# Optimization experiments

Hardware: AMD Instinct MI355X
Metric: run time of the kernel (lower is better)

Reference implementation:

```python
import jax, jax.numpy as jnp
import numpy as np

B, T, C = 8, 2048, 1024
NEG_BIG = -1e30  # exp(NEG_BIG - row_max) underflows to exactly 0 in fp32


def setup_inputs() -> dict:
    key = jax.random.key(0)
    k1, k2 = jax.random.split(key)
    x = jax.random.normal(k1, (B, T, C), dtype=jnp.float32)
    # nn.Linear weight, shape [out, in]; forward computes x @ W^T
    W_H = jax.random.normal(k2, (C, C), dtype=jnp.float32) * (1.0 / np.sqrt(C))
    return {"x": x, "W_H": W_H}


def reference(x, W_H):
    Tdim = x.shape[1]
    xH = jnp.einsum('btc,dc->btd', x, W_H)          # H(x) = x @ W^T, [B,T,C]
    scores = jnp.einsum('btc,bsc->bts', x, xH)       # bilinear scores, [B,T,T]
    # tril_plus_one=True -> strictly-lower-triangular mask (diagonal=-1)
    mask = jnp.tril(jnp.ones((Tdim, Tdim), dtype=bool), k=-1)
    scores = jnp.where(mask, scores, NEG_BIG)
    wei = jax.nn.softmax(scores, axis=-1)            # fully-masked rows -> uniform, zeroed below
    all_masked = ~mask.any(axis=-1)                  # [T], True for row 0
    wei = jnp.where(all_masked[None, :, None], 0.0, wei)
    out = jnp.einsum('bts,bsc->btc', wei, xH)
    return -out
```

## Files before the change

### kernel.cpp

```cpp
#include <hip/hip_runtime.h>
#include <stdint.h>

#define Bn 8
#define Tn 2048
#define Cn 1024
#define Mn (Bn * Tn)
#define NTRI 136

typedef __attribute__((ext_vector_type(4))) float f32x4;
typedef _Float16 f16;
typedef __attribute__((ext_vector_type(8))) _Float16 f16x8;
typedef uint16_t u16;
typedef uint32_t u32;

static __device__ __forceinline__ u16 f2h(float f) {
  union { f16 h; u16 u; } c; c.h = (f16)f; return c.u;
}
static __device__ __forceinline__ f32x4 mfmaH(f16x8 a, f16x8 b, f32x4 c) {
  return __builtin_amdgcn_mfma_f32_16x16x32_f16(a, b, c, 0, 0, 0);
}
static __device__ __forceinline__ void gld16(const void* g, void* l) {
  __builtin_amdgcn_global_load_lds(
      (const __attribute__((address_space(1))) u32*)g,
      (__attribute__((address_space(3))) u32*)l, 16, 0, 0);
}

__global__ __launch_bounds__(256) void ksplitW(const float* __restrict__ s,
                                               u16* __restrict__ hi) {
  size_t i = ((size_t)blockIdx.x * 256 + threadIdx.x) * 8;
  float4 a = *(const float4*)(s + i), b = *(const float4*)(s + i + 4);
  float f[8] = {a.x, a.y, a.z, a.w, b.x, b.y, b.z, b.w};
  union { u16 u[8]; uint4 v; } H;
#pragma unroll
  for (int j = 0; j < 8; ++j) H.u[j] = f2h(f[j]);
  *(uint4*)(hi + i) = H.v;
}

__global__ __launch_bounds__(256) void ksplitX(const float* __restrict__ s,
                                               u16* __restrict__ hi,
                                               u16* __restrict__ lo) {
  size_t i = ((size_t)blockIdx.x * 256 + threadIdx.x) * 8;
  float4 a = *(const float4*)(s + i), b = *(const float4*)(s + i + 4);
  float f[8] = {a.x, a.y, a.z, a.w, b.x, b.y, b.z, b.w};
  union { u16 u[8]; uint4 v; } H, L;
#pragma unroll
  for (int j = 0; j < 8; ++j) {
    f16 h = (f16)f[j];
    union { f16 h; u16 u; } ch; ch.h = h;
    H.u[j] = ch.u;
    L.u[j] = f2h(f[j] - (float)h);
  }
  *(uint4*)(hi + i) = H.v;
  *(uint4*)(lo + i) = L.v;
}

__global__ __launch_bounds__(256) void k1_xh(const u16* __restrict__ x_h,
                                             const u16* __restrict__ W_h,
                                             u16* __restrict__ xh) {
  __shared__ __align__(16) u16 Ah[8192], Bh[8192];
  const int tid = threadIdx.x;
  const int m0 = blockIdx.x * 128, n0 = blockIdx.y * 128;
  const int wave = tid >> 6, lane = tid & 63;
  const int wrow = (wave >> 1) * 64, wcol = (wave & 1) * 64;
  const int quad = lane >> 4, l16 = lane & 15;

  f32x4 acc[4][4] = {};

  for (int k0 = 0; k0 < Cn; k0 += 64) {
#pragma unroll
    for (int i = 0; i < 4; ++i) {
      int chunk = i * 256 + tid;
      int kk = chunk >> 9, row = (chunk >> 2) & 127, c8 = (chunk & 3) * 8;
      gld16(x_h + (size_t)(m0 + row) * Cn + k0 + kk * 32 + c8, Ah + chunk * 8);
      gld16(W_h + (size_t)(n0 + row) * Cn + k0 + kk * 32 + c8, Bh + chunk * 8);
    }
    __syncthreads();
#pragma unroll
    for (int kk = 0; kk < 2; ++kk) {
      f16x8 a[4], b[4];
#pragma unroll
      for (int i = 0; i < 4; ++i) {
        a[i] = *(const f16x8*)(Ah + kk * 4096 + (wrow + i * 16 + l16) * 32 + quad * 8);
        b[i] = *(const f16x8*)(Bh + kk * 4096 + (wcol + i * 16 + l16) * 32 + quad * 8);
      }
#pragma unroll
      for (int mi = 0; mi < 4; ++mi)
#pragma unroll
        for (int ni = 0; ni < 4; ++ni)
          acc[mi][ni] = mfmaH(a[mi], b[ni], acc[mi][ni]);
    }
    __syncthreads();
  }
#pragma unroll
  for (int mi = 0; mi < 4; ++mi)
#pragma unroll
    for (int ni = 0; ni < 4; ++ni)
#pragma unroll
      for (int r = 0; r < 4; ++r) {
        int row = wrow + mi * 16 + quad * 4 + r;
        int col = wcol + ni * 16 + l16;
        xh[(size_t)(m0 + row) * Cn + n0 + col] = f2h(acc[mi][ni][r]);
      }
}

__global__ __launch_bounds__(256) void k2_scores(const u16* __restrict__ x_h,
                                                 const u16* __restrict__ x_l,
                                                 const u16* __restrict__ xh,
                                                 u16* __restrict__ P,
                                                 float* __restrict__ mt,
                                                 float* __restrict__ lt) {
  __shared__ __align__(16) union {
    struct { u16 Ah[4096], Al[4096], Bh[4096]; } s;
    struct { float Mrow[2][128]; float Lrow[2][128]; } e;
  } u;
  const int tid = threadIdx.x;
  const int bL = blockIdx.y;
  const int lin = blockIdx.x;
  int qt = 0;
  while ((qt + 1) * (qt + 2) / 2 <= lin) qt++;
  const int st = lin - qt * (qt + 1) / 2;
  const int t0 = qt * 128, s0 = st * 128;
  const int wave = tid >> 6, lane = tid & 63;
  const int wrow = (wave >> 1) * 64, wcol = (wave & 1) * 64;
  const int quad = lane >> 4, l16 = lane & 15;
  const int srow = tid >> 2, skc = (tid & 3) * 8;

  f32x4 acc[4][4] = {};
  const size_t aoff = ((size_t)bL * Tn + t0 + srow) * Cn + skc;
  const size_t boff = ((size_t)bL * Tn + s0 + srow) * Cn + skc;

  for (int k0 = 0; k0 < Cn; k0 += 32) {
#pragma unroll
    for (int i = 0; i < 2; ++i) {
      size_t ro = (size_t)i * 64 * Cn;
      int lo_ = i * 2048 + tid * 8;
      gld16(x_h + aoff + ro + k0, u.s.Ah + lo_);
      gld16(x_l + aoff + ro + k0, u.s.Al + lo_);
      gld16(xh + boff + ro + k0, u.s.Bh + lo_);
    }
    __syncthreads();
    f16x8 a_h[4], a_l[4], b_h[4];
#pragma unroll
    for (int i = 0; i < 4; ++i) {
      a_h[i] = *(const f16x8*)(u.s.Ah + (wrow + i * 16 + l16) * 32 + quad * 8);
      a_l[i] = *(const f16x8*)(u.s.Al + (wrow + i * 16 + l16) * 32 + quad * 8);
      b_h[i] = *(const f16x8*)(u.s.Bh + (wcol + i * 16 + l16) * 32 + quad * 8);
    }
#pragma unroll
    for (int mi = 0; mi < 4; ++mi)
#pragma unroll
      for (int ni = 0; ni < 4; ++ni) {
        acc[mi][ni] = mfmaH(a_h[mi], b_h[ni], acc[mi][ni]);
        acc[mi][ni] = mfmaH(a_l[mi], b_h[ni], acc[mi][ni]);
      }
    __syncthreads();
  }

  float rm[4][4];
#pragma unroll
  for (int mi = 0; mi < 4; ++mi)
#pragma unroll
    for (int r = 0; r < 4; ++r) {
      int row = wrow + mi * 16 + quad * 4 + r;
      float m = -1e30f;
#pragma unroll
      for (int ni = 0; ni < 4; ++ni) {
        int col = wcol + ni * 16 + l16;
        if (s0 + col >= t0 + row) acc[mi][ni][r] = -1e30f;
        m = fmaxf(m, acc[mi][ni][r]);
      }
      m = fmaxf(m, __shfl_xor(m, 1));
      m = fmaxf(m, __shfl_xor(m, 2));
      m = fmaxf(m, __shfl_xor(m, 4));
      m = fmaxf(m, __shfl_xor(m, 8));
      rm[mi][r] = m;
    }
  if (l16 == 0) {
#pragma unroll
    for (int mi = 0; mi < 4; ++mi)
#pragma unroll
      for (int r = 0; r < 4; ++r)
        u.e.Mrow[wave & 1][wrow + mi * 16 + quad * 4 + r] = rm[mi][r];
  }
  __syncthreads();
  float rs[4][4];
#pragma unroll
  for (int mi = 0; mi < 4; ++mi)
#pragma unroll
    for (int r = 0; r < 4; ++r) {
      int row = wrow + mi * 16 + quad * 4 + r;
      float m2 = fmaxf(u.e.Mrow[0][row], u.e.Mrow[1][row]);
      float s = 0.f;
#pragma unroll
      for (int ni = 0; ni < 4; ++ni) {
        int col = wcol + ni * 16 + l16;
        float p = (s0 + col < t0 + row) ? __expf(acc[mi][ni][r] - m2) : 0.0f;
        acc[mi][ni][r] = p;
        s += p;
      }
      s += __shfl_xor(s, 1);
      s += __shfl_xor(s, 2);
      s += __shfl_xor(s, 4);
      s += __shfl_xor(s, 8);
      rs[mi][r] = s;
      rm[mi][r] = m2;
    }
  if (l16 == 0) {
#pragma unroll
    for (int mi = 0; mi < 4; ++mi)
#pragma unroll
      for (int r = 0; r < 4; ++r)
        u.e.Lrow[wave & 1][wrow + mi * 16 + quad * 4 + r] = rs[mi][r];
  }
  __syncthreads();
  if ((wave & 1) == 0 && l16 == 0) {
#pragma unroll
    for (int mi = 0; mi < 4; ++mi)
#pragma unroll
      for (int r = 0; r < 4; ++r) {
        int row = wrow + mi * 16 + quad * 4 + r;
        size_t rI = (size_t)bL * Tn + t0 + row;
        mt[rI * 16 + st] = rm[mi][r];
        lt[rI * 16 + st] = u.e.Lrow[0][row] + u.e.Lrow[1][row];
      }
  }
  const size_t pbase = (size_t)(bL * NTRI + lin) * 16384;
#pragma unroll
  for (int mi = 0; mi < 4; ++mi)
#pragma unroll
    for (int ni = 0; ni < 4; ++ni)
#pragma unroll
      for (int r = 0; r < 4; ++r) {
        int row = wrow + mi * 16 + quad * 4 + r;
        int col = wcol + ni * 16 + l16;
        P[pbase + row * 128 + col] = f2h(acc[mi][ni][r]);
      }
}

__global__ __launch_bounds__(256) void k3_stats(const float* __restrict__ mt,
                                                const float* __restrict__ lt,
                                                float* __restrict__ Mr,
                                                float* __restrict__ Li) {
  int r = blockIdx.x * 256 + threadIdx.x;
  int t = r & (Tn - 1);
  int nt = (t == 0) ? 0 : (((t - 1) >> 7) + 1);
  float M = -1e30f;
  for (int i = 0; i < nt; ++i) M = fmaxf(M, mt[(size_t)r * 16 + i]);
  float L = 0.f;
  for (int i = 0; i < nt; ++i) L += lt[(size_t)r * 16 + i] * __expf(mt[(size_t)r * 16 + i] - M);
  Mr[r] = M;
  Li[r] = (L > 0.f) ? 1.f / L : 0.f;
}

__global__ __launch_bounds__(256) void ktr(const u16* __restrict__ src,
                                           u16* __restrict__ dst) {
  __shared__ __align__(16) u16 S[128 * 136];
  const int t0 = blockIdx.x * 128, c0 = blockIdx.y * 128, b = blockIdx.z;
  const int tid = threadIdx.x;
#pragma unroll
  for (int i = 0; i < 8; ++i) {
    int chunk = tid + i * 256;
    int row = chunk >> 4, c8 = (chunk & 15) * 8;
    uint4 v = *(const uint4*)(src + ((size_t)b * Tn + t0 + row) * Cn + c0 + c8);
    *(uint4*)(S + row * 136 + c8) = v;
  }
  __syncthreads();
#pragma unroll
  for (int i = 0; i < 8; ++i) {
    int chunk = tid + i * 256;
    int crow = chunk >> 4, t8 = (chunk & 15) * 8;
    union { u16 s[8]; uint4 v; } o;
#pragma unroll
    for (int j = 0; j < 8; ++j) o.s[j] = S[(t8 + j) * 136 + crow];
    *(uint4*)(dst + ((size_t)b * Cn + c0 + crow) * Tn + t0 + t8) = o.v;
  }
}

__global__ __launch_bounds__(256) void k4_out(const u16* __restrict__ P,
                                              const u16* __restrict__ xhT,
                                              const float* __restrict__ mt,
                                              const float* __restrict__ Mr,
                                              const float* __restrict__ Li,
                                              float* __restrict__ out) {
  __shared__ __align__(16) u16 Ap[8192], Bp[8192];
  const int tid = threadIdx.x;
  const int tt = 15 - blockIdx.x;
  const int cn = blockIdx.y, bL = blockIdx.z;
  const int t0 = tt * 128, c0 = cn * 128;
  const int wave = tid >> 6, lane = tid & 63;
  const int wrow = (wave >> 1) * 64, wcol = (wave & 1) * 64;
  const int quad = lane >> 4, l16 = lane & 15;

  f32x4 acc[4][4] = {};
  size_t rI[4]; float MrL[4], LiL[4];
#pragma unroll
  for (int mi = 0; mi < 4; ++mi) {
    rI[mi] = (size_t)bL * Tn + t0 + wrow + mi * 16 + l16;
    MrL[mi] = Mr[rI[mi]];
    LiL[mi] = Li[rI[mi]];
  }
  const size_t bbase = ((size_t)bL * Cn + c0) * Tn;

  for (int st = 0; st <= tt; ++st) {
    f16 ah[4];
#pragma unroll
    for (int mi = 0; mi < 4; ++mi)
      ah[mi] = (f16)(__expf(mt[rI[mi] * 16 + st] - MrL[mi]) * LiL[mi]);
    const size_t pbase = (size_t)(bL * NTRI + tt * (tt + 1) / 2 + st) * 16384;
#pragma unroll 1
    for (int kl = 0; kl < 128; kl += 64) {
#pragma unroll
      for (int i = 0; i < 4; ++i) {
        int chunk = i * 256 + tid;
        int kk = chunk >> 9, row = (chunk >> 2) & 127, c8 = (chunk & 3) * 8;
        gld16(P + pbase + (size_t)row * 128 + kl + kk * 32 + c8, Ap + chunk * 8);
        gld16(xhT + bbase + (size_t)row * Tn + st * 128 + kl + kk * 32 + c8, Bp + chunk * 8);
      }
      __syncthreads();
#pragma unroll
      for (int kk = 0; kk < 2; ++kk) {
        f16x8 a[4], b[4];
#pragma unroll
        for (int i = 0; i < 4; ++i) {
          a[i] = *(const f16x8*)(Ap + kk * 4096 + (wrow + i * 16 + l16) * 32 + quad * 8);
          f16x8 sv;
#pragma unroll
          for (int j = 0; j < 8; ++j) sv[j] = ah[i];
          a[i] = a[i] * sv;
          b[i] = *(const f16x8*)(Bp + kk * 4096 + (wcol + i * 16 + l16) * 32 + quad * 8);
        }
#pragma unroll
        for (int mi = 0; mi < 4; ++mi)
#pragma unroll
          for (int ni = 0; ni < 4; ++ni)
            acc[mi][ni] = mfmaH(a[mi], b[ni], acc[mi][ni]);
      }
      __syncthreads();
    }
  }
#pragma unroll
  for (int mi = 0; mi < 4; ++mi)
#pragma unroll
    for (int ni = 0; ni < 4; ++ni)
#pragma unroll
      for (int r = 0; r < 4; ++r) {
        int row = wrow + mi * 16 + quad * 4 + r;
        int col = wcol + ni * 16 + l16;
        out[((size_t)bL * Tn + t0 + row) * Cn + c0 + col] = -acc[mi][ni][r];
      }
}

extern "C" void kernel_launch(void* const* d_in, const int* in_sizes, int n_in,
                              void* d_out, int out_size, void* d_ws, size_t ws_size,
                              hipStream_t stream) {
  (void)in_sizes; (void)n_in; (void)out_size;
  const float* x = (const float*)d_in[0];
  const float* W = (const float*)d_in[1];
  float* out = (float*)d_out;

  const size_t FULL_NEED = 3ull * Mn * Cn * 2 + (size_t)Bn * NTRI * 16384 * 2 +
                           (size_t)Cn * Cn * 2 + 2ull * Mn * 16 * 4 + 2ull * Mn * 4;
  const int nch = (ws_size >= FULL_NEED) ? 1 : 2;
  const int nb = Bn / nch;
  const size_t rowsC = (size_t)nb * Tn;
  const size_t sA = rowsC * Cn * 2;

  char* p = (char*)d_ws;
  u16* x_h = (u16*)p; p += sA;
  u16* xLT = (u16*)p; p += sA;
  u16* xh  = (u16*)p; p += sA;
  u16* Pp  = (u16*)p; p += (size_t)nb * NTRI * 16384 * 2;
  u16* W_h = (u16*)p; p += (size_t)Cn * Cn * 2;
  float* mt = (float*)p; p += rowsC * 16 * 4;
  float* lt = (float*)p; p += rowsC * 16 * 4;
  float* Mr = (float*)p; p += rowsC * 4;
  float* Li = (float*)p; p += rowsC * 4;

  dim3 blk(256);
  ksplitW<<<dim3(Cn * Cn / 2048), blk, 0, stream>>>(W, W_h);
  for (int c = 0; c < nch; ++c) {
    const float* xc = x + (size_t)c * rowsC * Cn;
    float* oc = out + (size_t)c * rowsC * Cn;
    ksplitX<<<dim3((u32)(rowsC * Cn / 2048)), blk, 0, stream>>>(xc, x_h, xLT);
    k1_xh<<<dim3((u32)(rowsC / 128), Cn / 128), blk, 0, stream>>>(x_h, W_h, xh);
    k2_scores<<<dim3(NTRI, nb), blk, 0, stream>>>(x_h, xLT, xh, Pp, mt, lt);
    k3_stats<<<dim3((u32)(rowsC / 256)), blk, 0, stream>>>(mt, lt, Mr, Li);
    ktr<<<dim3(Tn / 128, Cn / 128, nb), blk, 0, stream>>>(xh, xLT);
    k4_out<<<dim3(16, Cn / 128, nb), blk, 0, stream>>>(Pp, xLT, mt, Mr, Li, oc);
  }
}
```

Baseline: 427.6 us.

## Widen score kernel tiles to 128x256 with 512 threads sharing A loads

The causal score kernel now computes 128x256 tiles per block using 8 waves, so each query-row A tile (hi and lo halves) is loaded once for two 128-wide key blocks. This cuts redundant global and LDS traffic for A and reduces block count from 136 to 72 per batch. The cost is some wasted MFMA work on the upper 128-column half of diagonal tiles, which is computed and then discarded, plus higher per-block register and LDS pressure.

```diff
diff --git a/kernel.cpp b/kernel.cpp
--- a/kernel.cpp
+++ b/kernel.cpp
@@ -6,6 +6,7 @@
 #define Cn 1024
 #define Mn (Bn * Tn)
 #define NTRI 136
+#define NLIN2 72
 
 typedef __attribute__((ext_vector_type(4))) float f32x4;
 typedef _Float16 f16;
@@ -103,56 +104,58 @@
       }
 }
 
-__global__ __launch_bounds__(256) void k2_scores(const u16* __restrict__ x_h,
+__global__ __launch_bounds__(512) void k2_scores(const u16* __restrict__ x_h,
                                                  const u16* __restrict__ x_l,
                                                  const u16* __restrict__ xh,
                                                  u16* __restrict__ P,
                                                  float* __restrict__ mt,
                                                  float* __restrict__ lt) {
   __shared__ __align__(16) union {
-    struct { u16 Ah[4096], Al[4096], Bh[4096]; } s;
-    struct { float Mrow[2][128]; float Lrow[2][128]; } e;
+    struct { u16 Ah[4096], Al[4096], Bh[8192]; } s;
+    struct { float Mrow[4][128]; float Lrow[4][128]; } e;
   } u;
   const int tid = threadIdx.x;
   const int bL = blockIdx.y;
   const int lin = blockIdx.x;
-  int qt = 0;
-  while ((qt + 1) * (qt + 2) / 2 <= lin) qt++;
-  const int st = lin - qt * (qt + 1) / 2;
-  const int t0 = qt * 128, s0 = st * 128;
+  int qt = 0, cum = 0;
+  while (cum + ((qt >> 1) + 1) <= lin) { cum += (qt >> 1) + 1; qt++; }
+  const int bcol = lin - cum;
+  const int t0 = qt * 128, s0 = bcol * 256;
   const int wave = tid >> 6, lane = tid & 63;
-  const int wrow = (wave >> 1) * 64, wcol = (wave & 1) * 64;
+  const int wc = wave & 3;
+  const int wrow = (wave >> 2) * 64, wcol = wc * 64;
   const int quad = lane >> 4, l16 = lane & 15;
-  const int srow = tid >> 2, skc = (tid & 3) * 8;
 
   f32x4 acc[4][4] = {};
-  const size_t aoff = ((size_t)bL * Tn + t0 + srow) * Cn + skc;
-  const size_t boff = ((size_t)bL * Tn + s0 + srow) * Cn + skc;
+  const size_t abase = ((size_t)bL * Tn + t0) * Cn;
+  const size_t bbase = ((size_t)bL * Tn + s0) * Cn;
+  const int arow = tid >> 2, ac8 = (tid & 3) * 8;
 
   for (int k0 = 0; k0 < Cn; k0 += 32) {
+    size_t aoff = abase + (size_t)arow * Cn + k0 + ac8;
+    gld16(x_h + aoff, u.s.Ah + tid * 8);
+    gld16(x_l + aoff, u.s.Al + tid * 8);
 #pragma unroll
     for (int i = 0; i < 2; ++i) {
-      size_t ro = (size_t)i * 64 * Cn;
-      int lo_ = i * 2048 + tid * 8;
-      gld16(x_h + aoff + ro + k0, u.s.Ah + lo_);
-      gld16(x_l + aoff + ro + k0, u.s.Al + lo_);
-      gld16(xh + boff + ro + k0, u.s.Bh + lo_);
+      int ch = i * 512 + tid;
+      int row = ch >> 2, c8 = (ch & 3) * 8;
+      gld16(xh + bbase + (size_t)row * Cn + k0 + c8, u.s.Bh + ch * 8);
     }
     __syncthreads();
-    f16x8 a_h[4], a_l[4], b_h[4];
-#pragma unroll
-    for (int i = 0; i < 4; ++i) {
-      a_h[i] = *(const f16x8*)(u.s.Ah + (wrow + i * 16 + l16) * 32 + quad * 8);
-      a_l[i] = *(const f16x8*)(u.s.Al + (wrow + i * 16 + l16) * 32 + quad * 8);
-      b_h[i] = *(const f16x8*)(u.s.Bh + (wcol + i * 16 + l16) * 32 + quad * 8);
-    }
-#pragma unroll
-    for (int mi = 0; mi < 4; ++mi)
+    f16x8 b[4];
+#pragma unroll
+    for (int ni = 0; ni < 4; ++ni)
+      b[ni] = *(const f16x8*)(u.s.Bh + (wcol + ni * 16 + l16) * 32 + quad * 8);
+#pragma unroll
+    for (int mi = 0; mi < 4; ++mi) {
+      f16x8 ah = *(const f16x8*)(u.s.Ah + (wrow + mi * 16 + l16) * 32 + quad * 8);
+      f16x8 al = *(const f16x8*)(u.s.Al + (wrow + mi * 16 + l16) * 32 + quad * 8);
 #pragma unroll
       for (int ni = 0; ni < 4; ++ni) {
-        acc[mi][ni] = mfmaH(a_h[mi], b_h[ni], acc[mi][ni]);
-        acc[mi][ni] = mfmaH(a_l[mi], b_h[ni], acc[mi][ni]);
-      }
+        acc[mi][ni] = mfmaH(ah, b[ni], acc[mi][ni]);
+        acc[mi][ni] = mfmaH(al, b[ni], acc[mi][ni]);
+      }
+    }
     __syncthreads();
   }
 
@@ -165,8 +168,8 @@
       float m = -1e30f;
 #pragma unroll
       for (int ni = 0; ni < 4; ++ni) {
-        int col = wcol + ni * 16 + l16;
-        if (s0 + col >= t0 + row) acc[mi][ni][r] = -1e30f;
+        int scol = s0 + wcol + ni * 16 + l16;
+        if (scol >= t0 + row) acc[mi][ni][r] = -1e30f;
         m = fmaxf(m, acc[mi][ni][r]);
       }
       m = fmaxf(m, __shfl_xor(m, 1));
@@ -180,21 +183,22 @@
     for (int mi = 0; mi < 4; ++mi)
 #pragma unroll
       for (int r = 0; r < 4; ++r)
-        u.e.Mrow[wave & 1][wrow + mi * 16 + quad * 4 + r] = rm[mi][r];
+        u.e.Mrow[wc][wrow + mi * 16 + quad * 4 + r] = rm[mi][r];
   }
   __syncthreads();
+  const int h2 = (wc >> 1) * 2;
   float rs[4][4];
 #pragma unroll
   for (int mi = 0; mi < 4; ++mi)
 #pragma unroll
     for (int r = 0; r < 4; ++r) {
       int row = wrow + mi * 16 + quad * 4 + r;
-      float m2 = fmaxf(u.e.Mrow[0][row], u.e.Mrow[1][row]);
+      float m2 = fmaxf(u.e.Mrow[h2][row], u.e.Mrow[h2 + 1][row]);
       float s = 0.f;
 #pragma unroll
       for (int ni = 0; ni < 4; ++ni) {
-        int col = wcol + ni * 16 + l16;
-        float p = (s0 + col < t0 + row) ? __expf(acc[mi][ni][r] - m2) : 0.0f;
+        int scol = s0 + wcol + ni * 16 + l16;
+        float p = (scol < t0 + row) ? __expf(acc[mi][ni][r] - m2) : 0.0f;
         acc[mi][ni][r] = p;
         s += p;
       }
@@ -210,31 +214,34 @@
     for (int mi = 0; mi < 4; ++mi)
 #pragma unroll
       for (int r = 0; r < 4; ++r)
-        u.e.Lrow[wave & 1][wrow + mi * 16 + quad * 4 + r] = rs[mi][r];
+        u.e.Lrow[wc][wrow + mi * 16 + quad * 4 + r] = rs[mi][r];
   }
   __syncthreads();
-  if ((wave & 1) == 0 && l16 == 0) {
+  const int st128 = bcol * 2 + (wc >> 1);
+  if (st128 <= qt) {
+    if ((wc & 1) == 0 && l16 == 0) {
+#pragma unroll
+      for (int mi = 0; mi < 4; ++mi)
+#pragma unroll
+        for (int r = 0; r < 4; ++r) {
+          int row = wrow + mi * 16 + quad * 4 + r;
+          size_t rI = (size_t)bL * Tn + t0 + row;
+          mt[rI * 16 + st128] = rm[mi][r];
+          lt[rI * 16 + st128] = u.e.Lrow[wc][row] + u.e.Lrow[wc + 1][row];
+        }
+    }
+    const size_t pbase = (size_t)(bL * NTRI + qt * (qt + 1) / 2 + st128) * 16384;
 #pragma unroll
     for (int mi = 0; mi < 4; ++mi)
 #pragma unroll
-      for (int r = 0; r < 4; ++r) {
-        int row = wrow + mi * 16 + quad * 4 + r;
-        size_t rI = (size_t)bL * Tn + t0 + row;
-        mt[rI * 16 + st] = rm[mi][r];
-        lt[rI * 16 + st] = u.e.Lrow[0][row] + u.e.Lrow[1][row];
-      }
-  }
-  const size_t pbase = (size_t)(bL * NTRI + lin) * 16384;
-#pragma unroll
-  for (int mi = 0; mi < 4; ++mi)
-#pragma unroll
-    for (int ni = 0; ni < 4; ++ni)
-#pragma unroll
-      for (int r = 0; r < 4; ++r) {
-        int row = wrow + mi * 16 + quad * 4 + r;
-        int col = wcol + ni * 16 + l16;
-        P[pbase + row * 128 + col] = f2h(acc[mi][ni][r]);
-      }
+      for (int ni = 0; ni < 4; ++ni)
+#pragma unroll
+        for (int r = 0; r < 4; ++r) {
+          int row = wrow + mi * 16 + quad * 4 + r;
+          int pcol = (wcol & 64) + ni * 16 + l16;
+          P[pbase + row * 128 + pcol] = f2h(acc[mi][ni][r]);
+        }
+  }
 }
 
 __global__ __launch_bounds__(256) void k3_stats(const float* __restrict__ mt,
@@ -383,7 +390,7 @@
     float* oc = out + (size_t)c * rowsC * Cn;
     ksplitX<<<dim3((u32)(rowsC * Cn / 2048)), blk, 0, stream>>>(xc, x_h, xLT);
     k1_xh<<<dim3((u32)(rowsC / 128), Cn / 128), blk, 0, stream>>>(x_h, W_h, xh);
-    k2_scores<<<dim3(NTRI, nb), blk, 0, stream>>>(x_h, xLT, xh, Pp, mt, lt);
+    k2_scores<<<dim3(NLIN2, nb), dim3(512), 0, stream>>>(x_h, xLT, xh, Pp, mt, lt);
     k3_stats<<<dim3((u32)(rowsC / 256)), blk, 0, stream>>>(mt, lt, Mr, Li);
     ktr<<<dim3(Tn / 128, Cn / 128, nb), blk, 0, stream>>>(xh, xLT);
     k4_out<<<dim3(16, Cn / 128, nb), blk, 0, stream>>>(Pp, xLT, mt, Mr, Li, oc);
```

After: 435.3 us. Within noise of the previous version (+1.8%).
